# Optimization experiments

Measured on AMD Instinct MI355X. Metric: run time of the kernel, lower is better.

The kernel has to match this reference:

```python
import jax, jax.numpy as jnp
import numpy as np

B, T, I = 32768, 28, 28
H, C = 128, 10


def setup_inputs() -> dict:
    key = jax.random.key(0)
    ks = jax.random.split(key, 7)
    s_u = 1.0 / np.sqrt(I)
    s_w = 1.0 / np.sqrt(H)
    return {
        "x": jax.random.normal(ks[0], (B, T, I), dtype=jnp.float32),
        "U_w": jax.random.uniform(ks[1], (H, I), jnp.float32, -s_u, s_u),
        "U_b": jax.random.uniform(ks[2], (H,), jnp.float32, -s_u, s_u),
        "W_w": jax.random.uniform(ks[3], (H, H), jnp.float32, -s_w, s_w),
        "W_b": jax.random.uniform(ks[4], (H,), jnp.float32, -s_w, s_w),
        "V_w": jax.random.uniform(ks[5], (C, H), jnp.float32, -s_w, s_w),
        "V_b": jax.random.uniform(ks[6], (C,), jnp.float32, -s_w, s_w),
    }


def reference(x, U_w, U_b, W_w, W_b, V_w, V_b):
    # x: [B, T, I]. Precompute input projections for all timesteps at once
    # (one big GEMM), then scan the sequential recurrence on S.
    ux = jnp.einsum("bti,hi->tbh", x, U_w) + U_b  # [T, B, H]

    def step(S, ux_t):
        S = jnp.tanh(ux_t + S @ W_w.T + W_b)
        return S, None

    S0 = jnp.zeros((x.shape[0], W_w.shape[0]), dtype=x.dtype)
    S_final, _ = jax.lax.scan(step, S0, ux)
    return S_final @ V_w.T + V_b  # [B, C]
```

## Files before the change

kernel.cpp:

```cpp
#include <hip/hip_runtime.h>


#define T_STEPS 28
#define I_DIM   28
#define S_STRIDE 132

typedef __attribute__((ext_vector_type(4))) float f32x4;
typedef __attribute__((ext_vector_type(8))) short short8;

#define MFMA16 __builtin_amdgcn_mfma_f32_16x16x32_bf16

__device__ __forceinline__ unsigned pack2(float lo, float hi) {
#if __has_builtin(__builtin_amdgcn_cvt_pk_bf16_f32)
  auto p = __builtin_amdgcn_cvt_pk_bf16_f32(lo, hi);
  return __builtin_bit_cast(unsigned, p);
#else
  unsigned a = __builtin_bit_cast(unsigned, lo);
  a += 0x7FFFu + ((a >> 16) & 1u);
  unsigned b = __builtin_bit_cast(unsigned, hi);
  b += 0x7FFFu + ((b >> 16) & 1u);
  return (a >> 16) | (b & 0xFFFF0000u);
#endif
}

__device__ __forceinline__ float bf2f(unsigned short s) {
  return __builtin_bit_cast(float, (unsigned)s << 16);
}

__device__ __forceinline__ short8 to_frag(f32x4 a, f32x4 b) {
  union { unsigned u[4]; short8 v; } r;
  r.u[0] = pack2(a[0], a[1]);
  r.u[1] = pack2(a[2], a[3]);
  r.u[2] = pack2(b[0], b[1]);
  r.u[3] = pack2(b[2], b[3]);
  return r.v;
}

__device__ __forceinline__ short8 load_sfrag(const unsigned short* sp, int off) {
  union { uint2 d[2]; short8 v; } r;
  r.d[0] = *(const uint2*)(sp + off);
  r.d[1] = *(const uint2*)(sp + off + 4);
  return r.v;
}

__device__ __forceinline__ f32x4 tanh4(f32x4 z) {
  const float k = 2.8853900817779268f;
  f32x4 t = z * k;
  f32x4 e;
#pragma unroll
  for (int i = 0; i < 4; ++i) e[i] = __builtin_amdgcn_exp2f(t[i]);
  f32x4 d = e + 1.0f;
  f32x4 r;
#pragma unroll
  for (int i = 0; i < 4; ++i) r[i] = __builtin_amdgcn_rcpf(d[i]);
  return 1.0f - 2.0f * r;
}

__global__ __launch_bounds__(256, 4) void rnn_fused(
    const float* __restrict__ x,  const float* __restrict__ Uw,
    const float* __restrict__ Ub, const float* __restrict__ Ww,
    const float* __restrict__ Wb, const float* __restrict__ Vw,
    const float* __restrict__ Vb, float* __restrict__ out) {
  __shared__ __align__(16) unsigned short Sbuf[2][32 * S_STRIDE];

  const int tid  = threadIdx.x;
  const int w    = tid >> 6;
  const int lane = tid & 63;
  const int l15  = lane & 15;
  const int q    = lane >> 4;
  const int mrow = w * 32;
  const int b0   = blockIdx.x * 32;

  const f32x4 zero4 = {0.f, 0.f, 0.f, 0.f};

  short8 wfrag[2][4];
  short8 ufrag[2];
  f32x4  bias[2];
#pragma unroll
  for (int mt = 0; mt < 2; ++mt) {
    const int h = mrow + mt * 16 + l15;
    const float* wp = Ww + h * 128 + q * 8;
#pragma unroll
    for (int kt = 0; kt < 4; ++kt) {
      wfrag[mt][kt] = to_frag(*(const f32x4*)wp, *(const f32x4*)(wp + 4));
      wp += 32;
    }
    const float* up = Uw + h * I_DIM + q * 8;
    f32x4 u0 = *(const f32x4*)up;
    f32x4 u1 = zero4;
    if (q < 3) u1 = *(const f32x4*)(up + 4);
    ufrag[mt] = to_frag(u0, u1);
    const int hb = mrow + mt * 16 + q * 4;
    bias[mt] = *(const f32x4*)(Wb + hb) + *(const f32x4*)(Ub + hb);
  }

  const float* xlo[2];
  const float* xhi[2];
#pragma unroll
  for (int nt = 0; nt < 2; ++nt) {
    const float* base = x + (size_t)(b0 + nt * 16 + l15) * (T_STEPS * I_DIM);
    xlo[nt] = base + q * 8;
    xhi[nt] = base + ((q < 3) ? q * 8 + 4 : 0);
  }

  int ro[2];
#pragma unroll
  for (int nt = 0; nt < 2; ++nt) ro[nt] = (nt * 16 + l15) * S_STRIDE;

  f32x4 acc[2][2];

  {
    short8 xf[2];
#pragma unroll
    for (int nt = 0; nt < 2; ++nt) {
      f32x4 xa = *(const f32x4*)xlo[nt];
      f32x4 xb = *(const f32x4*)xhi[nt];
      xlo[nt] += I_DIM; xhi[nt] += I_DIM;
      xf[nt] = to_frag(xa, xb);
    }
    unsigned short* wp = &Sbuf[1][0];
#pragma unroll
    for (int mt = 0; mt < 2; ++mt)
#pragma unroll
      for (int nt = 0; nt < 2; ++nt) {
        f32x4 d = MFMA16(ufrag[mt], xf[nt], bias[mt], 0, 0, 0);
        f32x4 th = tanh4(d);
        uint2 dd; dd.x = pack2(th[0], th[1]); dd.y = pack2(th[2], th[3]);
        *(uint2*)(wp + ro[nt] + mrow + mt * 16 + q * 4) = dd;
      }
  }
  __syncthreads();

#pragma unroll 1
  for (int t = 1; t < T_STEPS; ++t) {
    f32x4 xa[2], xb[2];
#pragma unroll
    for (int nt = 0; nt < 2; ++nt) {
      xa[nt] = *(const f32x4*)xlo[nt];
      xb[nt] = *(const f32x4*)xhi[nt];
      xlo[nt] += I_DIM; xhi[nt] += I_DIM;
    }

    const unsigned short* sp = &Sbuf[t & 1][0];
#pragma unroll
    for (int mt = 0; mt < 2; ++mt)
#pragma unroll
      for (int nt = 0; nt < 2; ++nt) acc[mt][nt] = bias[mt];

#pragma unroll
    for (int kt = 0; kt < 4; ++kt) {
      short8 s0 = load_sfrag(sp, ro[0] + kt * 32 + q * 8);
      short8 s1 = load_sfrag(sp, ro[1] + kt * 32 + q * 8);
#pragma unroll
      for (int mt = 0; mt < 2; ++mt) {
        acc[mt][0] = MFMA16(wfrag[mt][kt], s0, acc[mt][0], 0, 0, 0);
        acc[mt][1] = MFMA16(wfrag[mt][kt], s1, acc[mt][1], 0, 0, 0);
      }
    }

    short8 xf0 = to_frag(xa[0], xb[0]);
    short8 xf1 = to_frag(xa[1], xb[1]);
#pragma unroll
    for (int mt = 0; mt < 2; ++mt) {
      acc[mt][0] = MFMA16(ufrag[mt], xf0, acc[mt][0], 0, 0, 0);
      acc[mt][1] = MFMA16(ufrag[mt], xf1, acc[mt][1], 0, 0, 0);
    }

    unsigned short* wp = &Sbuf[(t + 1) & 1][0];
#pragma unroll
    for (int mt = 0; mt < 2; ++mt)
#pragma unroll
      for (int nt = 0; nt < 2; ++nt) {
        f32x4 th = tanh4(acc[mt][nt]);
        uint2 dd; dd.x = pack2(th[0], th[1]); dd.y = pack2(th[2], th[3]);
        *(uint2*)(wp + ro[nt] + mrow + mt * 16 + q * 4) = dd;
      }
    __syncthreads();
  }

  {
    const unsigned short* sf = &Sbuf[0][0];
    const int r  = tid >> 3;
    const int c0 = tid & 7;
    const float* v0 = Vw + c0 * 128;
    const float* v1 = Vw + ((c0 & 1) + 8) * 128;
    const unsigned short* srow = sf + r * S_STRIDE;
    float a0 = 0.f, a1 = 0.f;
#pragma unroll 8
    for (int h = 0; h < 128; ++h) {
      float s = bf2f(srow[h]);
      a0 += s * v0[h];
      a1 += s * v1[h];
    }
    float* op = out + (size_t)(b0 + r) * 10;
    op[c0] = a0 + Vb[c0];
    if (c0 < 2) op[c0 + 8] = a1 + Vb[(c0 & 1) + 8];
  }
}

extern "C" void kernel_launch(void* const* d_in, const int* in_sizes, int n_in,
                              void* d_out, int out_size, void* d_ws, size_t ws_size,
                              hipStream_t stream) {
  const float* x  = (const float*)d_in[0];
  const float* Uw = (const float*)d_in[1];
  const float* Ub = (const float*)d_in[2];
  const float* Ww = (const float*)d_in[3];
  const float* Wb = (const float*)d_in[4];
  const float* Vw = (const float*)d_in[5];
  const float* Vb = (const float*)d_in[6];
  rnn_fused<<<1024, 256, 0, stream>>>(x, Uw, Ub, Ww, Wb, Vw, Vb, (float*)d_out);
}
```

Baseline: 216.1 us.

## Prefetch next-step x, widen LDS reads, use rational tanh approximation

```diff
diff --git a/kernel.cpp b/kernel.cpp
--- a/kernel.cpp
+++ b/kernel.cpp
@@ -3,10 +3,11 @@
 
 #define T_STEPS 28
 #define I_DIM   28
-#define S_STRIDE 132
+#define S_STRIDE 136
 
 typedef __attribute__((ext_vector_type(4))) float f32x4;
 typedef __attribute__((ext_vector_type(8))) short short8;
+typedef __attribute__((ext_vector_type(4))) unsigned int uint4v;
 
 #define MFMA16 __builtin_amdgcn_mfma_f32_16x16x32_bf16
 
@@ -37,23 +38,22 @@
 }
 
 __device__ __forceinline__ short8 load_sfrag(const unsigned short* sp, int off) {
-  union { uint2 d[2]; short8 v; } r;
-  r.d[0] = *(const uint2*)(sp + off);
-  r.d[1] = *(const uint2*)(sp + off + 4);
-  return r.v;
+  uint4v d = *(const uint4v*)(sp + off);
+  return __builtin_bit_cast(short8, d);
 }
 
 __device__ __forceinline__ f32x4 tanh4(f32x4 z) {
-  const float k = 2.8853900817779268f;
-  f32x4 t = z * k;
-  f32x4 e;
-#pragma unroll
-  for (int i = 0; i < 4; ++i) e[i] = __builtin_amdgcn_exp2f(t[i]);
-  f32x4 d = e + 1.0f;
+  f32x4 x2 = z * z;
+  f32x4 p = 945.0f + x2 * (105.0f + x2);
+  f32x4 q = 945.0f + x2 * (420.0f + 15.0f * x2);
+  f32x4 num = z * p;
   f32x4 r;
 #pragma unroll
-  for (int i = 0; i < 4; ++i) r[i] = __builtin_amdgcn_rcpf(d[i]);
-  return 1.0f - 2.0f * r;
+  for (int i = 0; i < 4; ++i) r[i] = __builtin_amdgcn_rcpf(q[i]);
+  f32x4 t = num * r;
+#pragma unroll
+  for (int i = 0; i < 4; ++i) t[i] = __builtin_amdgcn_fmed3f(t[i], -1.0f, 1.0f);
+  return t;
 }
 
 __global__ __launch_bounds__(256, 4) void rnn_fused(
@@ -108,58 +108,60 @@
   for (int nt = 0; nt < 2; ++nt) ro[nt] = (nt * 16 + l15) * S_STRIDE;
 
   f32x4 acc[2][2];
+  short8 xf0, xf1;
 
   {
-    short8 xf[2];
-#pragma unroll
-    for (int nt = 0; nt < 2; ++nt) {
-      f32x4 xa = *(const f32x4*)xlo[nt];
-      f32x4 xb = *(const f32x4*)xhi[nt];
-      xlo[nt] += I_DIM; xhi[nt] += I_DIM;
-      xf[nt] = to_frag(xa, xb);
-    }
+    f32x4 xa0 = *(const f32x4*)xlo[0], xb0 = *(const f32x4*)xhi[0];
+    f32x4 xa1 = *(const f32x4*)xlo[1], xb1 = *(const f32x4*)xhi[1];
+    xlo[0] += I_DIM; xhi[0] += I_DIM; xlo[1] += I_DIM; xhi[1] += I_DIM;
+    f32x4 pa0 = *(const f32x4*)xlo[0], pb0 = *(const f32x4*)xhi[0];
+    f32x4 pa1 = *(const f32x4*)xlo[1], pb1 = *(const f32x4*)xhi[1];
+
+    xf0 = to_frag(xa0, xb0); xf1 = to_frag(xa1, xb1);
     unsigned short* wp = &Sbuf[1][0];
 #pragma unroll
-    for (int mt = 0; mt < 2; ++mt)
-#pragma unroll
-      for (int nt = 0; nt < 2; ++nt) {
-        f32x4 d = MFMA16(ufrag[mt], xf[nt], bias[mt], 0, 0, 0);
-        f32x4 th = tanh4(d);
-        uint2 dd; dd.x = pack2(th[0], th[1]); dd.y = pack2(th[2], th[3]);
-        *(uint2*)(wp + ro[nt] + mrow + mt * 16 + q * 4) = dd;
-      }
+    for (int mt = 0; mt < 2; ++mt) {
+      f32x4 d0 = MFMA16(ufrag[mt], xf0, bias[mt], 0, 0, 0);
+      f32x4 d1 = MFMA16(ufrag[mt], xf1, bias[mt], 0, 0, 0);
+      f32x4 t0 = tanh4(d0), t1 = tanh4(d1);
+      uint2 dd0; dd0.x = pack2(t0[0], t0[1]); dd0.y = pack2(t0[2], t0[3]);
+      uint2 dd1; dd1.x = pack2(t1[0], t1[1]); dd1.y = pack2(t1[2], t1[3]);
+      *(uint2*)(wp + ro[0] + mrow + mt * 16 + q * 4) = dd0;
+      *(uint2*)(wp + ro[1] + mrow + mt * 16 + q * 4) = dd1;
+    }
+    xf0 = to_frag(pa0, pb0); xf1 = to_frag(pa1, pb1);
   }
   __syncthreads();
 
 #pragma unroll 1
   for (int t = 1; t < T_STEPS; ++t) {
-    f32x4 xa[2], xb[2];
-#pragma unroll
-    for (int nt = 0; nt < 2; ++nt) {
-      xa[nt] = *(const f32x4*)xlo[nt];
-      xb[nt] = *(const f32x4*)xhi[nt];
-      xlo[nt] += I_DIM; xhi[nt] += I_DIM;
+    f32x4 pa0, pb0, pa1, pb1;
+    const bool more = (t < T_STEPS - 1);
+    if (more) {
+      xlo[0] += I_DIM; xhi[0] += I_DIM; xlo[1] += I_DIM; xhi[1] += I_DIM;
+      pa0 = *(const f32x4*)xlo[0]; pb0 = *(const f32x4*)xhi[0];
+      pa1 = *(const f32x4*)xlo[1]; pb1 = *(const f32x4*)xhi[1];
     }
 
     const unsigned short* sp = &Sbuf[t & 1][0];
-#pragma unroll
-    for (int mt = 0; mt < 2; ++mt)
-#pragma unroll
-      for (int nt = 0; nt < 2; ++nt) acc[mt][nt] = bias[mt];
-
-#pragma unroll
-    for (int kt = 0; kt < 4; ++kt) {
-      short8 s0 = load_sfrag(sp, ro[0] + kt * 32 + q * 8);
-      short8 s1 = load_sfrag(sp, ro[1] + kt * 32 + q * 8);
+
+    short8 sA = load_sfrag(sp, ro[0] + q * 8);
+    short8 sB = load_sfrag(sp, ro[1] + q * 8);
+#pragma unroll
+    for (int mt = 0; mt < 2; ++mt) {
+      acc[mt][0] = MFMA16(wfrag[mt][0], sA, bias[mt], 0, 0, 0);
+      acc[mt][1] = MFMA16(wfrag[mt][0], sB, bias[mt], 0, 0, 0);
+    }
+#pragma unroll
+    for (int kt = 1; kt < 4; ++kt) {
+      sA = load_sfrag(sp, ro[0] + kt * 32 + q * 8);
+      sB = load_sfrag(sp, ro[1] + kt * 32 + q * 8);
 #pragma unroll
       for (int mt = 0; mt < 2; ++mt) {
-        acc[mt][0] = MFMA16(wfrag[mt][kt], s0, acc[mt][0], 0, 0, 0);
-        acc[mt][1] = MFMA16(wfrag[mt][kt], s1, acc[mt][1], 0, 0, 0);
+        acc[mt][0] = MFMA16(wfrag[mt][kt], sA, acc[mt][0], 0, 0, 0);
+        acc[mt][1] = MFMA16(wfrag[mt][kt], sB, acc[mt][1], 0, 0, 0);
       }
     }
-
-    short8 xf0 = to_frag(xa[0], xb[0]);
-    short8 xf1 = to_frag(xa[1], xb[1]);
 #pragma unroll
     for (int mt = 0; mt < 2; ++mt) {
       acc[mt][0] = MFMA16(ufrag[mt], xf0, acc[mt][0], 0, 0, 0);
@@ -175,6 +177,8 @@
         uint2 dd; dd.x = pack2(th[0], th[1]); dd.y = pack2(th[2], th[3]);
         *(uint2*)(wp + ro[nt] + mrow + mt * 16 + q * 4) = dd;
       }
+
+    if (more) { xf0 = to_frag(pa0, pb0); xf1 = to_frag(pa1, pb1); }
     __syncthreads();
   }
 
```

Result: faster. 204.9 us (-5.2%).
